# Kernel optimization log

Measured on AMD Instinct MI355X. Metric: run time of the kernel, lower is better.

The kernel has to match this reference:

```python
import jax, jax.numpy as jnp
import numpy as np

N = 50000      # nodes
E = 600000     # edges
DIN = 128      # dim_in
DOUT = 128     # dim_out (mulhead=1)
DG = 64        # dim_gate


def setup_inputs() -> dict:
    key = jax.random.key(0)
    ks = jax.random.split(key, 10)
    rows = jax.random.randint(ks[0], (E,), 0, N, dtype=jnp.int32)   # dest nodes
    cols = jax.random.randint(ks[1], (E,), 0, N, dtype=jnp.int32)   # src nodes
    vals = jax.random.uniform(ks[2], (E,), dtype=jnp.float32)       # adj_norm values
    feat = jax.random.normal(ks[3], (N, DIN), dtype=jnp.float32)
    s = 1.0 / np.sqrt(DIN)
    W0 = jax.random.normal(ks[4], (DIN, DOUT), dtype=jnp.float32) * s
    b0 = jnp.zeros((DOUT,), dtype=jnp.float32)
    W1 = jax.random.normal(ks[5], (DIN, DOUT), dtype=jnp.float32) * s
    b1 = jnp.zeros((DOUT,), dtype=jnp.float32)
    att = jax.random.normal(ks[6], (2 * DOUT,), dtype=jnp.float32) * 0.1  # attention param [1, 2*DOUT] flattened
    W_pool = jax.random.normal(ks[7], (DIN, DG), dtype=jnp.float32) * s    # weight_pool_gate
    W_gate = jax.random.normal(ks[8], (2 * DIN + DG, 1), dtype=jnp.float32) * 0.05  # weight_gate, mulhead=1
    offset0 = jnp.zeros((DOUT,), dtype=jnp.float32)
    scale0 = jnp.ones((DOUT,), dtype=jnp.float32)
    offset1 = jnp.zeros((DOUT,), dtype=jnp.float32)
    scale1 = jnp.ones((DOUT,), dtype=jnp.float32)
    return dict(rows=rows, cols=cols, vals=vals, feat=feat, W0=W0, b0=b0,
                W1=W1, b1=b1, att=att, W_pool=W_pool, W_gate=W_gate,
                offset0=offset0, scale0=scale0, offset1=offset1, scale1=scale1)


def _batch_norm(x, scale, offset):
    # per-node norm over the feature dim (unbiased=False), matching _batch_norm
    m = x.mean(axis=1, keepdims=True)
    v = x.var(axis=1, keepdims=True) + 1e-9
    return (x - m) * scale * jax.lax.rsqrt(v) + offset


def reference(rows, cols, vals, feat, W0, b0, W1, b1, att, W_pool, W_gate,
              offset0, scale0, offset1, scale1):
    n = feat.shape[0]
    d = W0.shape[1]
    # --- gate value (GaAN eq. 3) ---
    zj = feat @ W_pool                                   # [N, DG]
    neigh_zj = jax.ops.segment_max(zj[cols], rows, num_segments=n)  # per-row max over neighbors
    neigh_zj = jnp.where(jnp.isfinite(neigh_zj), neigh_zj, 0.0)     # empty rows -> zeros
    neigh_mean = jax.ops.segment_sum(vals[:, None] * feat[cols], rows, num_segments=n)  # spmm(adj, feat)
    gate = jnp.concatenate([feat, neigh_zj, neigh_mean], axis=1) @ W_gate  # [N, 1]
    # --- per-order feature transforms (order=1, mulhead=1) ---
    h0 = jax.nn.relu(feat @ W0 + b0)                     # order 0 (self)
    h1 = jax.nn.relu(feat @ W1 + b1)                     # order 1 (neighbor)
    # --- sparse attention aggregation ---
    a_self = jax.nn.leaky_relu(h0 @ att[:d], 0.2)        # [N]
    a_neigh = jax.nn.leaky_relu(h1 @ att[d:], 0.2)       # [N]
    e = a_self[rows] + a_neigh[cols]                     # per-edge score (replaces adj values)
    agg = jax.ops.segment_sum(e[:, None] * h1[cols], rows, num_segments=n)  # spmm(att_adj, h1)
    agg = agg * gate[:, :1]                              # gated
    # --- per-node batch norm, then 'mean' aggregation (sum of orders) ---
    return _batch_norm(h0, scale0, offset0) + _batch_norm(agg, scale1, offset1)
```

## Files before the change

kernel.cpp:

```cpp
#include <hip/hip_runtime.h>

#define DIN 128
#define DG 64

typedef __attribute__((ext_vector_type(8))) short short8;
typedef __attribute__((ext_vector_type(4))) float f32x4;

static __device__ __forceinline__ unsigned short f2bf(float x) {
    unsigned u = __builtin_bit_cast(unsigned, x);
    u = (u + 0x7FFF + ((u >> 16) & 1)) >> 16;
    return (unsigned short)u;
}
static __device__ __forceinline__ float bf2f(unsigned short s) {
    return __builtin_bit_cast(float, (unsigned)s << 16);
}

__global__ void k_deg_wt(const int* __restrict__ rows, int* __restrict__ deg,
                         int* __restrict__ slot, int E, int nDeg,
                         const float* __restrict__ W0, const float* __restrict__ W1,
                         unsigned short* __restrict__ Bt) {
    int b = blockIdx.x;
    if (b < nDeg) {
        int e = b * 256 + threadIdx.x;
        if (e < E) slot[e] = atomicAdd(&deg[rows[e]], 1);
    } else {
        int k = b - nDeg;
        int c = threadIdx.x;
        const float* W = (c < 128) ? W0 : W1;
        Bt[c * 128 + k] = f2bf(W[k * 128 + (c & 127)]);
    }
}

__global__ __launch_bounds__(1024) void k_scan1(const int* __restrict__ deg,
                                                int* __restrict__ rowptr,
                                                int* __restrict__ bsum, int n) {
    __shared__ int wsum[16];
    __shared__ int woff[16];
    int tid = threadIdx.x;
    int lane = tid & 63, w = tid >> 6;
    int i = blockIdx.x * 1024 + tid;
    int v = (i < n) ? deg[i] : 0;
    int x = v;
    #pragma unroll
    for (int off = 1; off < 64; off <<= 1) {
        int y = __shfl_up(x, off, 64);
        if (lane >= off) x += y;
    }
    if (lane == 63) wsum[w] = x;
    __syncthreads();
    if (w == 0) {
        int t = (lane < 16) ? wsum[lane] : 0;
        int xx = t;
        #pragma unroll
        for (int off = 1; off < 16; off <<= 1) {
            int y = __shfl_up(xx, off, 64);
            if (lane >= off) xx += y;
        }
        if (lane < 16) woff[lane] = xx - t;
    }
    __syncthreads();
    if (i < n) rowptr[i] = x - v + woff[w];
    if (tid == 1023) bsum[blockIdx.x] = woff[15] + wsum[15];
}

#define AS_LD 132
#define ALD 136
#define SMEM_BYTES 25088

static __device__ __forceinline__ void zj_body(
    const float* __restrict__ feat, const float* __restrict__ Wp,
    const float* __restrict__ Wg,
    float* __restrict__ zj, float* __restrict__ gpart, float* __restrict__ fdotg,
    int N, char* smem) {
    float* As = (float*)smem;
    float* Bs = (float*)(smem + 32 * AS_LD * 4);
    int tid = threadIdx.x;
    int tx = tid & 15, ty = tid >> 4;
    int m0 = blockIdx.x * 128;
    if (m0 >= N) return;
    float acc[8][4];
    #pragma unroll
    for (int r = 0; r < 8; ++r)
        #pragma unroll
        for (int c = 0; c < 4; ++c) acc[r][c] = 0.f;
    float gdot[8], fdot[8];
    #pragma unroll
    for (int r = 0; r < 8; ++r) { gdot[r] = 0.f; fdot[r] = 0.f; }
    for (int kc = 0; kc < 128; kc += 32) {
        for (int i = tid; i < 1024; i += 256) {
            int m = i >> 3, kq = (i & 7) << 2;
            int node = m0 + m;
            float4 f;
            if (node < N) f = *(const float4*)&feat[(size_t)node * 128 + kc + kq];
            else          f = make_float4(0.f, 0.f, 0.f, 0.f);
            As[(kq + 0) * AS_LD + m] = f.x;
            As[(kq + 1) * AS_LD + m] = f.y;
            As[(kq + 2) * AS_LD + m] = f.z;
            As[(kq + 3) * AS_LD + m] = f.w;
        }
        for (int i = tid; i < 512; i += 256) {
            int k = i >> 4, cq = (i & 15) << 2;
            *(float4*)&Bs[k * 64 + cq] = *(const float4*)&Wp[(size_t)(kc + k) * 64 + cq];
        }
        __syncthreads();
        #pragma unroll 8
        for (int kk = 0; kk < 32; ++kk) {
            const float* ar = &As[kk * AS_LD];
            float4 a0 = *(const float4*)(ar + 4 * tx);
            float4 a1 = *(const float4*)(ar + 64 + 4 * tx);
            float4 b0v = *(const float4*)&Bs[kk * 64 + 4 * ty];
            float a[8] = {a0.x, a0.y, a0.z, a0.w, a1.x, a1.y, a1.z, a1.w};
            #pragma unroll
            for (int r = 0; r < 8; ++r) {
                acc[r][0] += a[r] * b0v.x; acc[r][1] += a[r] * b0v.y;
                acc[r][2] += a[r] * b0v.z; acc[r][3] += a[r] * b0v.w;
            }
            float g1 = Wg[kc + kk];
            float g2 = Wg[192 + kc + kk];
            #pragma unroll
            for (int r = 0; r < 8; ++r) { gdot[r] += a[r] * g1; fdot[r] += a[r] * g2; }
        }
        __syncthreads();
    }
    #pragma unroll
    for (int r = 0; r < 8; ++r) {
        int node = m0 + ((r < 4) ? (4 * tx + r) : (64 + 4 * tx + (r - 4)));
        if (node >= N) continue;
        *(float4*)&zj[(size_t)node * 64 + 4 * ty] =
            make_float4(acc[r][0], acc[r][1], acc[r][2], acc[r][3]);
        if (ty == 0) { gpart[node] = gdot[r]; fdotg[node] = fdot[r]; }
    }
}

static __device__ __forceinline__ void mfma_body(
    const float* __restrict__ feat, const unsigned short* __restrict__ Bt,
    const float* __restrict__ b0, const float* __restrict__ b1,
    const float* __restrict__ att,
    float* __restrict__ h0, unsigned short* __restrict__ hb,
    float* __restrict__ a_self, float* __restrict__ a_neigh, int N, char* smem) {
    unsigned short* As = (unsigned short*)smem;
    float* sredA = (float*)(smem + 64 * ALD * 2);
    float* nredA = sredA + 128;
    int tid = threadIdx.x;
    int m0 = blockIdx.x * 64;
    for (int i = tid; i < 2048; i += 256) {
        int row = i >> 5, ch = i & 31;
        int node = m0 + row;
        float4 f;
        if (node < N) f = *(const float4*)&feat[(size_t)node * 128 + ch * 4];
        else          f = make_float4(0.f, 0.f, 0.f, 0.f);
        unsigned p0 = (unsigned)f2bf(f.x) | ((unsigned)f2bf(f.y) << 16);
        unsigned p1 = (unsigned)f2bf(f.z) | ((unsigned)f2bf(f.w) << 16);
        *(uint2*)&As[row * ALD + ch * 4] = make_uint2(p0, p1);
    }
    __syncthreads();
    int w = tid >> 6, lane = tid & 63;
    int lm = lane & 15, q = lane >> 4;
    f32x4 acc[4][4];
    #pragma unroll
    for (int rt = 0; rt < 4; ++rt)
        #pragma unroll
        for (int ct = 0; ct < 4; ++ct)
            #pragma unroll
            for (int r = 0; r < 4; ++r) acc[rt][ct][r] = 0.f;
    #pragma unroll
    for (int ks = 0; ks < 4; ++ks) {
        short8 a[4], b[4];
        #pragma unroll
        for (int rt = 0; rt < 4; ++rt)
            a[rt] = *(const short8*)&As[(rt * 16 + lm) * ALD + ks * 32 + q * 8];
        #pragma unroll
        for (int ct = 0; ct < 4; ++ct)
            b[ct] = *(const short8*)&Bt[(size_t)(w * 64 + ct * 16 + lm) * 128 + ks * 32 + q * 8];
        #pragma unroll
        for (int rt = 0; rt < 4; ++rt)
            #pragma unroll
            for (int ct = 0; ct < 4; ++ct)
                acc[rt][ct] = __builtin_amdgcn_mfma_f32_16x16x32_bf16(a[rt], b[ct], acc[rt][ct], 0, 0, 0);
    }
    float sacc[4][4];
    #pragma unroll
    for (int rt = 0; rt < 4; ++rt)
        #pragma unroll
        for (int r = 0; r < 4; ++r) sacc[rt][r] = 0.f;
    #pragma unroll
    for (int ct = 0; ct < 4; ++ct) {
        int col = w * 64 + ct * 16 + lm;
        float attc = att[col];
        float bias = (w < 2) ? b0[col] : b1[col - 128];
        #pragma unroll
        for (int rt = 0; rt < 4; ++rt) {
            #pragma unroll
            for (int r = 0; r < 4; ++r) {
                float v = acc[rt][ct][r] + bias;
                v = fmaxf(v, 0.f);
                sacc[rt][r] += v * attc;
                int node = m0 + rt * 16 + q * 4 + r;
                if (node < N) {
                    if (w < 2) h0[(size_t)node * 128 + col] = v;
                    else       hb[(size_t)node * 128 + (col - 128)] = f2bf(v);
                }
            }
        }
    }
    float* red = (w < 2) ? sredA : nredA;
    #pragma unroll
    for (int rt = 0; rt < 4; ++rt)
        #pragma unroll
        for (int r = 0; r < 4; ++r) {
            float s = sacc[rt][r];
            s += __shfl_xor(s, 1, 64); s += __shfl_xor(s, 2, 64);
            s += __shfl_xor(s, 4, 64); s += __shfl_xor(s, 8, 64);
            if (lm == 0) red[(w & 1) * 64 + rt * 16 + q * 4 + r] = s;
        }
    __syncthreads();
    if (tid < 64) {
        int node = m0 + tid;
        if (node < N) {
            float s  = sredA[tid] + sredA[64 + tid];
            float nn = nredA[tid] + nredA[64 + tid];
            a_self[node]  = (s  >= 0.f) ? s  : 0.2f * s;
            a_neigh[node] = (nn >= 0.f) ? nn : 0.2f * nn;
        }
    }
}

static __device__ __forceinline__ void scanfin_body(
    int* __restrict__ rowptr, const int* __restrict__ bsum, int nbs, int n) {
    int b = blockIdx.x;
    int i = b * 256 + threadIdx.x;
    if (b * 256 > n) return;
    int seg = (b * 256) >> 10;
    int pref = 0;
    for (int t = 0; t < seg; ++t) pref += bsum[t];
    if (i < n) rowptr[i] += pref;
    else if (i == n) {
        int tot = pref;
        for (int t = seg; t < nbs; ++t) tot += bsum[t];
        rowptr[n] = tot;
    }
}

__global__ __launch_bounds__(256) void k_fused(
    const float* __restrict__ feat, const float* __restrict__ Wp,
    const unsigned short* __restrict__ Bt,
    const float* __restrict__ b0, const float* __restrict__ b1,
    const float* __restrict__ att, const float* __restrict__ Wg,
    float* __restrict__ h0, unsigned short* __restrict__ hb,
    float* __restrict__ zj, float* __restrict__ gpart, float* __restrict__ fdotg,
    float* __restrict__ a_self, float* __restrict__ a_neigh,
    int* __restrict__ rowptr, const int* __restrict__ bsum, int nbs, int nsc, int N) {
    __shared__ __align__(16) char smem[SMEM_BYTES];
    if (blockIdx.y == 0)
        zj_body(feat, Wp, Wg, zj, gpart, fdotg, N, smem);
    else if (blockIdx.y == 1)
        mfma_body(feat, Bt, b0, b1, att, h0, hb, a_self, a_neigh, N, smem);
    else if (blockIdx.x < nsc)
        scanfin_body(rowptr, bsum, nbs, N);
}

__global__ void k_scatter_meta(const int* __restrict__ rows, const int* __restrict__ cols,
                               const float* __restrict__ vals,
                               const int* __restrict__ rowptr, const int* __restrict__ slot,
                               const float* __restrict__ a_neigh, const float* __restrict__ fdotg,
                               float4* __restrict__ meta, int E) {
    int e = blockIdx.x * blockDim.x + threadIdx.x;
    if (e < E) {
        int c = cols[e];
        int dst = rowptr[rows[e]] + slot[e];
        meta[dst] = make_float4(__builtin_bit_cast(float, c),
                                a_neigh[c], vals[e] * fdotg[c], 0.f);
    }
}

template<int C>
static __device__ __forceinline__ void agg_chunk_m(
    const float4* __restrict__ meta, int j, int je, int E, int lane, float asr,
    const unsigned short* __restrict__ hb, const float* __restrict__ zj,
    float2& acca, float& zmax, float& vfsum) {
    float4 m[C]; bool act[C];
    #pragma unroll
    for (int t = 0; t < C; ++t) {
        int jj = j + t;
        act[t] = jj < je;
        m[t] = meta[min(jj, E - 1)];
    }
    ushort2 hv[C]; float zv[C];
    #pragma unroll
    for (int t = 0; t < C; ++t) {
        int c = __builtin_bit_cast(int, m[t].x);
        hv[t] = ((const ushort2*)(hb + (size_t)c * 128))[lane];
        zv[t] = zj[(size_t)c * 64 + lane];
    }
    #pragma unroll
    for (int t = 0; t < C; ++t) {
        float es = act[t] ? (asr + m[t].y) : 0.f;
        acca.x += es * bf2f(hv[t].x);
        acca.y += es * bf2f(hv[t].y);
        zmax = fmaxf(zmax, act[t] ? zv[t] : -__builtin_inff());
        vfsum += act[t] ? m[t].z : 0.f;
    }
}

__global__ __launch_bounds__(256) void k_aggregate(
    const float4* __restrict__ meta, const int* __restrict__ rowptr,
    const float* __restrict__ h0, const unsigned short* __restrict__ hb,
    const float* __restrict__ zj,
    const float* __restrict__ a_self, const float* __restrict__ gpart,
    const float* __restrict__ Wg,
    const float* __restrict__ scale0, const float* __restrict__ offset0,
    const float* __restrict__ scale1, const float* __restrict__ offset1,
    float* __restrict__ out, int N, int E) {
    int r = blockIdx.x * 4 + (threadIdx.x >> 6);
    int lane = threadIdx.x & 63;
    if (r >= N) return;
    int jb = rowptr[r], je = rowptr[r + 1];
    float asr = a_self[r];
    float gp  = gpart[r];
    float wgl = Wg[128 + lane];
    float2 x0 = ((const float2*)(h0 + (size_t)r * 128))[lane];
    float2 sc0 = ((const float2*)scale0)[lane], of0 = ((const float2*)offset0)[lane];
    float2 sc1 = ((const float2*)scale1)[lane], of1 = ((const float2*)offset1)[lane];
    float2 acca = {0.f, 0.f};
    float zmax = -__builtin_inff();
    float vfsum = 0.f;
    agg_chunk_m<16>(meta, jb, je, E, lane, asr, hb, zj, acca, zmax, vfsum);
    for (int j = jb + 16; j < je; j += 8)
        agg_chunk_m<8>(meta, j, je, E, lane, asr, hb, zj, acca, zmax, vfsum);
    if (jb == je) zmax = 0.f;
    float gs = zmax * wgl;
    #pragma unroll
    for (int off = 32; off; off >>= 1) gs += __shfl_xor(gs, off, 64);
    float gate = gp + gs + vfsum;
    float2 ag = {acca.x * gate, acca.y * gate};
    float m0s = x0.x + x0.y;
    #pragma unroll
    for (int off = 32; off; off >>= 1) m0s += __shfl_xor(m0s, off, 64);
    float m0 = m0s * (1.f / 128.f);
    float d0x = x0.x - m0, d0y = x0.y - m0;
    float v0s = d0x * d0x + d0y * d0y;
    #pragma unroll
    for (int off = 32; off; off >>= 1) v0s += __shfl_xor(v0s, off, 64);
    float inv0 = rsqrtf(v0s * (1.f / 128.f) + 1e-9f);
    float m1s = ag.x + ag.y;
    #pragma unroll
    for (int off = 32; off; off >>= 1) m1s += __shfl_xor(m1s, off, 64);
    float m1 = m1s * (1.f / 128.f);
    float d1x = ag.x - m1, d1y = ag.y - m1;
    float v1s = d1x * d1x + d1y * d1y;
    #pragma unroll
    for (int off = 32; off; off >>= 1) v1s += __shfl_xor(v1s, off, 64);
    float inv1 = rsqrtf(v1s * (1.f / 128.f) + 1e-9f);
    float2 o;
    o.x = d0x * sc0.x * inv0 + of0.x + d1x * sc1.x * inv1 + of1.x;
    o.y = d0y * sc0.y * inv0 + of0.y + d1y * sc1.y * inv1 + of1.y;
    ((float2*)(out + (size_t)r * 128))[lane] = o;
}

extern "C" void kernel_launch(void* const* d_in, const int* in_sizes, int n_in,
                              void* d_out, int out_size, void* d_ws, size_t ws_size,
                              hipStream_t stream) {
    const int*   rows   = (const int*)d_in[0];
    const int*   cols   = (const int*)d_in[1];
    const float* vals   = (const float*)d_in[2];
    const float* feat   = (const float*)d_in[3];
    const float* W0     = (const float*)d_in[4];
    const float* b0     = (const float*)d_in[5];
    const float* W1     = (const float*)d_in[6];
    const float* b1     = (const float*)d_in[7];
    const float* att    = (const float*)d_in[8];
    const float* Wp     = (const float*)d_in[9];
    const float* Wg     = (const float*)d_in[10];
    const float* offset0 = (const float*)d_in[11];
    const float* scale0  = (const float*)d_in[12];
    const float* offset1 = (const float*)d_in[13];
    const float* scale1  = (const float*)d_in[14];
    float* out = (float*)d_out;

    const int E = in_sizes[0];
    const int N = in_sizes[3] / DIN;
    const int Npad = (N + 63) & ~63;

    char* ws = (char*)d_ws;
    float* h0          = (float*)ws;          ws += (size_t)N * 128 * sizeof(float);
    unsigned short* hb = (unsigned short*)ws; ws += (size_t)N * 128 * sizeof(unsigned short);
    float* zj          = (float*)ws;          ws += (size_t)N * 64 * sizeof(float);
    unsigned short* Bt = (unsigned short*)ws; ws += (size_t)256 * 128 * sizeof(unsigned short);
    float* a_self  = (float*)ws; ws += (size_t)N * sizeof(float);
    float* a_neigh = (float*)ws; ws += (size_t)N * sizeof(float);
    float* gpart   = (float*)ws; ws += (size_t)N * sizeof(float);
    float* fdotg   = (float*)ws; ws += (size_t)N * sizeof(float);
    int* deg      = (int*)ws; ws += (size_t)(N + 1) * sizeof(int);
    int* rowptr   = (int*)ws; ws += (size_t)(N + 1) * sizeof(int);
    int* bsum     = (int*)ws; ws += 64 * sizeof(int);
    int* slot     = (int*)ws; ws += (size_t)E * sizeof(int);
    ws = (char*)(((size_t)ws + 15) & ~(size_t)15);
    float4* meta  = (float4*)ws; ws += (size_t)E * sizeof(float4);

    hipMemsetAsync(deg, 0, (size_t)(N + 1) * sizeof(int), stream);

    int nDeg = (E + 255) / 256;
    k_deg_wt<<<nDeg + 128, 256, 0, stream>>>(rows, deg, slot, E, nDeg, W0, W1, Bt);

    int nb = (N + 1023) >> 10;
    k_scan1<<<nb, 1024, 0, stream>>>(deg, rowptr, bsum, N);

    int nsc = (N + 256) / 256;
    dim3 gg(Npad / 64, 3);
    k_fused<<<gg, 256, 0, stream>>>(feat, Wp, Bt, b0, b1, att, Wg,
                                    h0, hb, zj, gpart, fdotg, a_self, a_neigh,
                                    rowptr, bsum, nb, nsc, N);

    k_scatter_meta<<<nDeg, 256, 0, stream>>>(rows, cols, vals, rowptr, slot,
                                             a_neigh, fdotg, meta, E);

    int nb4 = (N + 3) / 4;
    k_aggregate<<<nb4, 256, 0, stream>>>(meta, rowptr, h0, hb, zj,
                                         a_self, gpart, Wg,
                                         scale0, offset0, scale1, offset1, out, N, E);
}
```

Baseline: 265.5 us.

## Split each row's edge aggregation across two wavefronts with LDS reduction

The aggregation kernel now assigns two wavefronts per destination row instead of one, each handling alternating 8-edge chunks, and combines their partial sums, max and gate terms through shared memory before the normalization epilogue. The aim is more memory-level parallelism for the gather-bound neighbor loop, since rows average about 12 edges. The cost is a block-wide barrier, LDS traffic, twice as many wavefronts, and an idle second wave during the epilogue. The initial 16-edge chunk is dropped in favour of uniform 8-edge chunks.

```diff
diff --git a/kernel.cpp b/kernel.cpp
--- a/kernel.cpp
+++ b/kernel.cpp
@@ -311,28 +311,35 @@
     const float* __restrict__ scale0, const float* __restrict__ offset0,
     const float* __restrict__ scale1, const float* __restrict__ offset1,
     float* __restrict__ out, int N, int E) {
-    int r = blockIdx.x * 4 + (threadIdx.x >> 6);
-    int lane = threadIdx.x & 63;
-    if (r >= N) return;
-    int jb = rowptr[r], je = rowptr[r + 1];
-    float asr = a_self[r];
-    float gp  = gpart[r];
-    float wgl = Wg[128 + lane];
-    float2 x0 = ((const float2*)(h0 + (size_t)r * 128))[lane];
-    float2 sc0 = ((const float2*)scale0)[lane], of0 = ((const float2*)offset0)[lane];
-    float2 sc1 = ((const float2*)scale1)[lane], of1 = ((const float2*)offset1)[lane];
+    __shared__ float ls[2][2][256];
+    int tid = threadIdx.x;
+    int pr = tid >> 7;
+    int h  = (tid >> 6) & 1;
+    int lane = tid & 63;
+    int r = blockIdx.x * 2 + pr;
+    bool valid = r < N;
+    int jb = 0, je = 0;
+    float asr = 0.f;
+    if (valid) { jb = rowptr[r]; je = rowptr[r + 1]; asr = a_self[r]; }
     float2 acca = {0.f, 0.f};
     float zmax = -__builtin_inff();
     float vfsum = 0.f;
-    agg_chunk_m<16>(meta, jb, je, E, lane, asr, hb, zj, acca, zmax, vfsum);
-    for (int j = jb + 16; j < je; j += 8)
+    for (int j = jb + 8 * h; j < je; j += 16)
         agg_chunk_m<8>(meta, j, je, E, lane, asr, hb, zj, acca, zmax, vfsum);
+    *(float4*)&ls[pr][h][lane * 4] = make_float4(acca.x, acca.y, zmax, vfsum);
+    __syncthreads();
+    if (h == 1 || !valid) return;
+    float4 o1 = *(const float4*)&ls[pr][1][lane * 4];
+    acca.x += o1.x; acca.y += o1.y;
+    zmax = fmaxf(zmax, o1.z);
+    vfsum += o1.w;
     if (jb == je) zmax = 0.f;
-    float gs = zmax * wgl;
+    float gs = zmax * Wg[128 + lane];
     #pragma unroll
     for (int off = 32; off; off >>= 1) gs += __shfl_xor(gs, off, 64);
-    float gate = gp + gs + vfsum;
+    float gate = gpart[r] + gs + vfsum;
     float2 ag = {acca.x * gate, acca.y * gate};
+    float2 x0 = ((const float2*)(h0 + (size_t)r * 128))[lane];
     float m0s = x0.x + x0.y;
     #pragma unroll
     for (int off = 32; off; off >>= 1) m0s += __shfl_xor(m0s, off, 64);
@@ -351,6 +358,8 @@
     #pragma unroll
     for (int off = 32; off; off >>= 1) v1s += __shfl_xor(v1s, off, 64);
     float inv1 = rsqrtf(v1s * (1.f / 128.f) + 1e-9f);
+    float2 sc0 = ((const float2*)scale0)[lane], of0 = ((const float2*)offset0)[lane];
+    float2 sc1 = ((const float2*)scale1)[lane], of1 = ((const float2*)offset1)[lane];
     float2 o;
     o.x = d0x * sc0.x * inv0 + of0.x + d1x * sc1.x * inv1 + of1.x;
     o.y = d0y * sc0.y * inv0 + of0.y + d1y * sc1.y * inv1 + of1.y;
@@ -414,8 +423,8 @@
     k_scatter_meta<<<nDeg, 256, 0, stream>>>(rows, cols, vals, rowptr, slot,
                                              a_neigh, fdotg, meta, E);
 
-    int nb4 = (N + 3) / 4;
-    k_aggregate<<<nb4, 256, 0, stream>>>(meta, rowptr, h0, hb, zj,
+    int nb2 = (N + 1) / 2;
+    k_aggregate<<<nb2, 256, 0, stream>>>(meta, rowptr, h0, hb, zj,
                                          a_self, gpart, Wg,
                                          scale0, offset0, scale1, offset1, out, N, E);
 }
```

After: 257.1 us. 3.2% less time.

## Replace two-pass scan with single-pass decoupled-lookback scan inside fused kernel

Applied to the files above, without the earlier changes.

Removes the separate k_scan1 launch and instead performs the row-pointer prefix sum inside the fused kernel's third grid slice. Each block scans 1024 degrees and chains block prefixes through decoupled lookback on a flag/value array, which is zeroed by the same memset as deg. This saves one kernel launch and a dependency barrier. The aggregate kernel also drops its 16-wide first chunk in favour of a uniform 8-wide loop, clamps meta loads to the row's own range, and defers scale/offset loads until after the edge loop to ease register pressure. The lookback spins on earlier blocks, so it relies on those blocks being scheduled; with only about 49 scan blocks this should be safe.

```diff
diff --git a/kernel.cpp b/kernel.cpp
--- a/kernel.cpp
+++ b/kernel.cpp
@@ -15,10 +15,10 @@
     return __builtin_bit_cast(float, (unsigned)s << 16);
 }
 
-__global__ void k_deg_wt(const int* __restrict__ rows, int* __restrict__ deg,
-                         int* __restrict__ slot, int E, int nDeg,
-                         const float* __restrict__ W0, const float* __restrict__ W1,
-                         unsigned short* __restrict__ Bt) {
+__global__ void k_pre(const int* __restrict__ rows, int* __restrict__ deg,
+                      int* __restrict__ slot, int E, int nDeg,
+                      const float* __restrict__ W0, const float* __restrict__ W1,
+                      unsigned short* __restrict__ Bt) {
     int b = blockIdx.x;
     if (b < nDeg) {
         int e = b * 256 + threadIdx.x;
@@ -29,38 +29,6 @@
         const float* W = (c < 128) ? W0 : W1;
         Bt[c * 128 + k] = f2bf(W[k * 128 + (c & 127)]);
     }
-}
-
-__global__ __launch_bounds__(1024) void k_scan1(const int* __restrict__ deg,
-                                                int* __restrict__ rowptr,
-                                                int* __restrict__ bsum, int n) {
-    __shared__ int wsum[16];
-    __shared__ int woff[16];
-    int tid = threadIdx.x;
-    int lane = tid & 63, w = tid >> 6;
-    int i = blockIdx.x * 1024 + tid;
-    int v = (i < n) ? deg[i] : 0;
-    int x = v;
-    #pragma unroll
-    for (int off = 1; off < 64; off <<= 1) {
-        int y = __shfl_up(x, off, 64);
-        if (lane >= off) x += y;
-    }
-    if (lane == 63) wsum[w] = x;
-    __syncthreads();
-    if (w == 0) {
-        int t = (lane < 16) ? wsum[lane] : 0;
-        int xx = t;
-        #pragma unroll
-        for (int off = 1; off < 16; off <<= 1) {
-            int y = __shfl_up(xx, off, 64);
-            if (lane >= off) xx += y;
-        }
-        if (lane < 16) woff[lane] = xx - t;
-    }
-    __syncthreads();
-    if (i < n) rowptr[i] = x - v + woff[w];
-    if (tid == 1023) bsum[blockIdx.x] = woff[15] + wsum[15];
 }
 
 #define AS_LD 132
@@ -225,20 +193,66 @@
     }
 }
 
-static __device__ __forceinline__ void scanfin_body(
-    int* __restrict__ rowptr, const int* __restrict__ bsum, int nbs, int n) {
+static __device__ __forceinline__ void scan_body(
+    const int* __restrict__ deg, int* __restrict__ rowptr,
+    unsigned long long* __restrict__ bstate, int n, int nbs, char* smem) {
     int b = blockIdx.x;
-    int i = b * 256 + threadIdx.x;
-    if (b * 256 > n) return;
-    int seg = (b * 256) >> 10;
-    int pref = 0;
-    for (int t = 0; t < seg; ++t) pref += bsum[t];
-    if (i < n) rowptr[i] += pref;
-    else if (i == n) {
-        int tot = pref;
-        for (int t = seg; t < nbs; ++t) tot += bsum[t];
-        rowptr[n] = tot;
-    }
+    if (b >= nbs) return;
+    int* wsum = (int*)smem;
+    int* bprefs = (int*)smem + 8;
+    int tid = threadIdx.x, lane = tid & 63, w = tid >> 6;
+    int base = b * 1024 + tid * 4;
+    int4 v = make_int4(0, 0, 0, 0);
+    if (base + 3 < n) v = *(const int4*)&deg[base];
+    else {
+        if (base     < n) v.x = deg[base];
+        if (base + 1 < n) v.y = deg[base + 1];
+        if (base + 2 < n) v.z = deg[base + 2];
+        if (base + 3 < n) v.w = deg[base + 3];
+    }
+    int s = v.x + v.y + v.z + v.w;
+    int x = s;
+    #pragma unroll
+    for (int off = 1; off < 64; off <<= 1) {
+        int y = __shfl_up(x, off, 64);
+        if (lane >= off) x += y;
+    }
+    if (lane == 63) wsum[w] = x;
+    __syncthreads();
+    int wpref = 0;
+    for (int t = 0; t < w; ++t) wpref += wsum[t];
+    int btotal = wsum[0] + wsum[1] + wsum[2] + wsum[3];
+    int excl = x - s + wpref;
+    if (tid == 0) {
+        unsigned long long pack =
+            ((unsigned long long)(b == 0 ? 2u : 1u) << 32) | (unsigned)btotal;
+        atomicExch(&bstate[b], pack);
+        int pref = 0;
+        if (b > 0) {
+            int i = b - 1;
+            while (i >= 0) {
+                unsigned long long st = atomicAdd(&bstate[i], 0ULL);
+                unsigned f = (unsigned)(st >> 32);
+                if (f == 0) { __builtin_amdgcn_s_sleep(1); continue; }
+                pref += (int)(st & 0xffffffffULL);
+                if (f == 2) break;
+                --i;
+            }
+            atomicExch(&bstate[b], (2ULL << 32) | (unsigned)(pref + btotal));
+        }
+        bprefs[0] = pref;
+    }
+    __syncthreads();
+    int p = bprefs[0] + excl;
+    if (base + 3 < n) {
+        *(int4*)&rowptr[base] = make_int4(p, p + v.x, p + v.x + v.y, p + v.x + v.y + v.z);
+    } else {
+        if (base     < n) rowptr[base]     = p;
+        if (base + 1 < n) rowptr[base + 1] = p + v.x;
+        if (base + 2 < n) rowptr[base + 2] = p + v.x + v.y;
+        if (base + 3 < n) rowptr[base + 3] = p + v.x + v.y + v.z;
+    }
+    if (b == nbs - 1 && tid == 0) rowptr[n] = bprefs[0] + btotal;
 }
 
 __global__ __launch_bounds__(256) void k_fused(
@@ -249,14 +263,15 @@
     float* __restrict__ h0, unsigned short* __restrict__ hb,
     float* __restrict__ zj, float* __restrict__ gpart, float* __restrict__ fdotg,
     float* __restrict__ a_self, float* __restrict__ a_neigh,
-    int* __restrict__ rowptr, const int* __restrict__ bsum, int nbs, int nsc, int N) {
+    const int* __restrict__ deg, int* __restrict__ rowptr,
+    unsigned long long* __restrict__ bstate, int nbs, int N) {
     __shared__ __align__(16) char smem[SMEM_BYTES];
     if (blockIdx.y == 0)
         zj_body(feat, Wp, Wg, zj, gpart, fdotg, N, smem);
     else if (blockIdx.y == 1)
         mfma_body(feat, Bt, b0, b1, att, h0, hb, a_self, a_neigh, N, smem);
-    else if (blockIdx.x < nsc)
-        scanfin_body(rowptr, bsum, nbs, N);
+    else
+        scan_body(deg, rowptr, bstate, N, nbs, smem);
 }
 
 __global__ void k_scatter_meta(const int* __restrict__ rows, const int* __restrict__ cols,
@@ -275,15 +290,16 @@
 
 template<int C>
 static __device__ __forceinline__ void agg_chunk_m(
-    const float4* __restrict__ meta, int j, int je, int E, int lane, float asr,
+    const float4* __restrict__ meta, int j, int je, int lane, float asr,
     const unsigned short* __restrict__ hb, const float* __restrict__ zj,
     float2& acca, float& zmax, float& vfsum) {
+    int jclamp = (je > 0) ? (je - 1) : 0;
     float4 m[C]; bool act[C];
     #pragma unroll
     for (int t = 0; t < C; ++t) {
         int jj = j + t;
         act[t] = jj < je;
-        m[t] = meta[min(jj, E - 1)];
+        m[t] = meta[act[t] ? jj : jclamp];
     }
     ushort2 hv[C]; float zv[C];
     #pragma unroll
@@ -310,29 +326,24 @@
     const float* __restrict__ Wg,
     const float* __restrict__ scale0, const float* __restrict__ offset0,
     const float* __restrict__ scale1, const float* __restrict__ offset1,
-    float* __restrict__ out, int N, int E) {
+    float* __restrict__ out, int N) {
     int r = blockIdx.x * 4 + (threadIdx.x >> 6);
     int lane = threadIdx.x & 63;
     if (r >= N) return;
     int jb = rowptr[r], je = rowptr[r + 1];
-    float asr = a_self[r];
-    float gp  = gpart[r];
-    float wgl = Wg[128 + lane];
-    float2 x0 = ((const float2*)(h0 + (size_t)r * 128))[lane];
-    float2 sc0 = ((const float2*)scale0)[lane], of0 = ((const float2*)offset0)[lane];
-    float2 sc1 = ((const float2*)scale1)[lane], of1 = ((const float2*)offset1)[lane];
     float2 acca = {0.f, 0.f};
     float zmax = -__builtin_inff();
     float vfsum = 0.f;
-    agg_chunk_m<16>(meta, jb, je, E, lane, asr, hb, zj, acca, zmax, vfsum);
-    for (int j = jb + 16; j < je; j += 8)
-        agg_chunk_m<8>(meta, j, je, E, lane, asr, hb, zj, acca, zmax, vfsum);
+    float asr = a_self[r];
+    for (int j = jb; j < je; j += 8)
+        agg_chunk_m<8>(meta, j, je, lane, asr, hb, zj, acca, zmax, vfsum);
     if (jb == je) zmax = 0.f;
-    float gs = zmax * wgl;
+    float gs = zmax * Wg[128 + lane];
     #pragma unroll
     for (int off = 32; off; off >>= 1) gs += __shfl_xor(gs, off, 64);
-    float gate = gp + gs + vfsum;
+    float gate = gpart[r] + gs + vfsum;
     float2 ag = {acca.x * gate, acca.y * gate};
+    float2 x0 = ((const float2*)(h0 + (size_t)r * 128))[lane];
     float m0s = x0.x + x0.y;
     #pragma unroll
     for (int off = 32; off; off >>= 1) m0s += __shfl_xor(m0s, off, 64);
@@ -351,6 +362,8 @@
     #pragma unroll
     for (int off = 32; off; off >>= 1) v1s += __shfl_xor(v1s, off, 64);
     float inv1 = rsqrtf(v1s * (1.f / 128.f) + 1e-9f);
+    float2 sc0 = ((const float2*)scale0)[lane], of0 = ((const float2*)offset0)[lane];
+    float2 sc1 = ((const float2*)scale1)[lane], of1 = ((const float2*)offset1)[lane];
     float2 o;
     o.x = d0x * sc0.x * inv0 + of0.x + d1x * sc1.x * inv1 + of1.x;
     o.y = d0y * sc0.y * inv0 + of0.y + d1y * sc1.y * inv1 + of1.y;
@@ -390,26 +403,24 @@
     float* a_neigh = (float*)ws; ws += (size_t)N * sizeof(float);
     float* gpart   = (float*)ws; ws += (size_t)N * sizeof(float);
     float* fdotg   = (float*)ws; ws += (size_t)N * sizeof(float);
+    ws = (char*)(((size_t)ws + 7) & ~(size_t)7);
+    unsigned long long* bstate = (unsigned long long*)ws; ws += 64 * sizeof(unsigned long long);
     int* deg      = (int*)ws; ws += (size_t)(N + 1) * sizeof(int);
     int* rowptr   = (int*)ws; ws += (size_t)(N + 1) * sizeof(int);
-    int* bsum     = (int*)ws; ws += 64 * sizeof(int);
     int* slot     = (int*)ws; ws += (size_t)E * sizeof(int);
     ws = (char*)(((size_t)ws + 15) & ~(size_t)15);
     float4* meta  = (float4*)ws; ws += (size_t)E * sizeof(float4);
 
-    hipMemsetAsync(deg, 0, (size_t)(N + 1) * sizeof(int), stream);
+    hipMemsetAsync(bstate, 0, 64 * sizeof(unsigned long long) + (size_t)(N + 1) * sizeof(int), stream);
 
     int nDeg = (E + 255) / 256;
-    k_deg_wt<<<nDeg + 128, 256, 0, stream>>>(rows, deg, slot, E, nDeg, W0, W1, Bt);
-
-    int nb = (N + 1023) >> 10;
-    k_scan1<<<nb, 1024, 0, stream>>>(deg, rowptr, bsum, N);
-
-    int nsc = (N + 256) / 256;
+    k_pre<<<nDeg + 128, 256, 0, stream>>>(rows, deg, slot, E, nDeg, W0, W1, Bt);
+
+    int nbs = (N + 1023) >> 10;
     dim3 gg(Npad / 64, 3);
     k_fused<<<gg, 256, 0, stream>>>(feat, Wp, Bt, b0, b1, att, Wg,
                                     h0, hb, zj, gpart, fdotg, a_self, a_neigh,
-                                    rowptr, bsum, nb, nsc, N);
+                                    deg, rowptr, bstate, nbs, N);
 
     k_scatter_meta<<<nDeg, 256, 0, stream>>>(rows, cols, vals, rowptr, slot,
                                              a_neigh, fdotg, meta, E);
@@ -417,5 +428,5 @@
     int nb4 = (N + 3) / 4;
     k_aggregate<<<nb4, 256, 0, stream>>>(meta, rowptr, h0, hb, zj,
                                          a_self, gpart, Wg,
-                                         scale0, offset0, scale1, offset1, out, N, E);
-}
+                                         scale0, offset0, scale1, offset1, out, N);
+}
```

Result: faster. 248.8 us (-6.3%).
